# Optimization experiments

Measured on AMD Instinct MI355X. Metric: run time of the kernel, lower is better.

The kernel has to match this reference:

```python
import jax, jax.numpy as jnp
import numpy as np

B, N, E, H = 4, 512, 512, 8
HD = E // H // 2            # 32; per-head value dim is 2*HD = 64
C_IN = 64                   # u_proj Conv2d in_channels
LAMBDA_INIT = 0.8 - 0.6 * float(np.exp(-0.3 * (28.0 / 28.0) * (1 - 1)))  # layer_idx=1, depth=28 -> 0.2
LN_EPS = 1e-5


def setup_inputs() -> dict:
    key = jax.random.key(0)
    ks = jax.random.split(key, 13)
    x = jax.random.normal(ks[0], (B, N, E), dtype=jnp.float32)
    u = jax.random.normal(ks[1], (B, N, N, C_IN), dtype=jnp.float32)
    umask = jax.random.randint(ks[2], (B, N, N, 2 * H), 0, 2).astype(bool)
    s = 0.02
    v_w = jax.random.normal(ks[3], (E, E), dtype=jnp.float32) * s        # nn.Linear weight [out,in]
    out_w = jax.random.normal(ks[4], (E, E), dtype=jnp.float32) * s
    uproj_w = jax.random.normal(ks[5], (2 * H, C_IN), dtype=jnp.float32) * s  # 1x1 conv kernel
    uproj_b = jax.random.normal(ks[6], (2 * H,), dtype=jnp.float32) * s
    lq1 = jax.random.normal(ks[7], (E,), dtype=jnp.float32) * 0.1
    lk1 = jax.random.normal(ks[8], (E,), dtype=jnp.float32) * 0.1
    lq2 = jax.random.normal(ks[9], (E,), dtype=jnp.float32) * 0.1
    lk2 = jax.random.normal(ks[10], (E,), dtype=jnp.float32) * 0.1
    ln_w = jnp.ones((2 * HD,), dtype=jnp.float32)
    ln_b = jnp.zeros((2 * HD,), dtype=jnp.float32)
    return {"x": x, "u": u, "umask": umask, "v_w": v_w, "out_w": out_w,
            "uproj_w": uproj_w, "uproj_b": uproj_b,
            "lq1": lq1, "lk1": lk1, "lq2": lq2, "lk2": lk2,
            "ln_w": ln_w, "ln_b": ln_b}


def reference(x, u, umask, v_w, out_w, uproj_w, uproj_b, lq1, lk1, lq2, lk2, ln_w, ln_b):
    b, n, e = x.shape
    # v projection -> [B, H, N, 2*HD]
    v = jnp.einsum('bne,fe->bnf', x, v_w).reshape(b, n, H, 2 * HD).transpose(0, 2, 1, 3)
    # 1x1 conv on u: [B,N,N,C_IN] -> [B,N,N,2H]
    ue = jnp.einsum('bnmc,hc->bnmh', u, uproj_w) + uproj_b
    ue = jnp.where(umask, -jnp.inf, ue)
    # transpose(3,1): [B,N,N,2H] -> [B,2H,N,N]; softmax over last (key) axis
    aw = jax.nn.softmax(jnp.transpose(ue, (0, 3, 2, 1)), axis=-1)
    lam1 = jnp.exp(jnp.sum(lq1 * lk1))
    lam2 = jnp.exp(jnp.sum(lq2 * lk2))
    lam = lam1 - lam2 + LAMBDA_INIT
    aw = aw.reshape(b, H, 2, n, n)
    diff = aw[:, :, 0] - lam * aw[:, :, 1]          # [B,H,N,N]
    attn = jnp.einsum('bhnm,bhmd->bhnd', diff, v)   # [B,H,N,2HD]
    # sub-LayerNorm over last dim
    mu = jnp.mean(attn, axis=-1, keepdims=True)
    var = jnp.mean(jnp.square(attn - mu), axis=-1, keepdims=True)
    attn = (attn - mu) * jax.lax.rsqrt(var + LN_EPS) * ln_w + ln_b
    attn = attn.transpose(0, 2, 1, 3).reshape(b, n, e)
    return jnp.einsum('bne,fe->bnf', attn, out_w)
```

## Files before the change

### kernel.cpp

```cpp
#include <hip/hip_runtime.h>
#include <math.h>

typedef _Float16 f16x8 __attribute__((ext_vector_type(8)));
typedef _Float16 f16x4 __attribute__((ext_vector_type(4)));
typedef float    f32x4 __attribute__((ext_vector_type(4)));

constexpr int kB  = 4;
constexpr int kN  = 512;
constexpr int kE  = 512;
constexpr int kH  = 8;
constexpr int kH2 = 16;
constexpr int kC  = 64;
constexpr int kDV = 64;
constexpr float kLamInit = 0.2f;

__global__ __launch_bounds__(256) void prep2_kernel(
    const float* __restrict__ x, const float* __restrict__ vw,
    const float* __restrict__ ow, const int* __restrict__ umask,
    const float* __restrict__ lq1, const float* __restrict__ lk1,
    const float* __restrict__ lq2, const float* __restrict__ lk2,
    _Float16* __restrict__ x16, _Float16* __restrict__ w16v,
    _Float16* __restrict__ w16o, unsigned short* __restrict__ mbits,
    float* __restrict__ lam_out) {
  const int bid = blockIdx.x;
  if (bid < 1536) {
    const float* src; _Float16* dst; int base;
    if (bid < 1024)      { src = x;  dst = x16;  base = bid; }
    else if (bid < 1280) { src = vw; dst = w16v; base = bid - 1024; }
    else                 { src = ow; dst = w16o; base = bid - 1280; }
    const int i = base * 256 + threadIdx.x;
    const float4 v = ((const float4*)src)[i];
    union { _Float16 h[4]; uint2 u2; } P;
    P.h[0]=(_Float16)v.x; P.h[1]=(_Float16)v.y;
    P.h[2]=(_Float16)v.z; P.h[3]=(_Float16)v.w;
    *(uint2*)(dst + i * 4) = P.u2;
  } else if (bid == 1536) {
    if (threadIdx.x < 64) {
      float s1 = 0.f, s2 = 0.f;
      for (int i = threadIdx.x; i < kE; i += 64) { s1 += lq1[i]*lk1[i]; s2 += lq2[i]*lk2[i]; }
      #pragma unroll
      for (int o = 32; o; o >>= 1) { s1 += __shfl_xor(s1, o); s2 += __shfl_xor(s2, o); }
      if (threadIdx.x == 0) lam_out[0] = expf(s1) - expf(s2) + kLamInit;
    }
  } else {
    const int i = (bid - 1537) * 256 + threadIdx.x;
    const int4* src = (const int4*)(umask + (size_t)i * kH2);
    unsigned int w = 0;
    #pragma unroll
    for (int c = 0; c < 4; ++c) {
      const int4 m = src[c];
      w |= (m.x & 1) << (c * 4 + 0);
      w |= (m.y & 1) << (c * 4 + 1);
      w |= (m.z & 1) << (c * 4 + 2);
      w |= (m.w & 1) << (c * 4 + 3);
    }
    mbits[i] = (unsigned short)w;
  }
}

__global__ __launch_bounds__(256, 4) void hgemm16f2(const _Float16* __restrict__ A16,
                                                    const _Float16* __restrict__ W16,
                                                    float* __restrict__ C,
                                                    int M, int F, int K) {
  const int tid = threadIdx.x, lane = tid & 63, wv = tid >> 6;
  const int l15 = lane & 15, l4 = lane >> 4;
  const int m0 = blockIdx.y * 16;
  const int f0 = blockIdx.x * 64 + wv * 16;
  f32x4 acc = {0, 0, 0, 0};
  const _Float16* Ap = A16 + (size_t)(m0 + l15) * K + l4 * 8;
  const _Float16* Wp = W16 + (size_t)(f0 + l15) * K + l4 * 8;
  for (int k0 = 0; k0 < K; k0 += 32) {
    const f16x8 af = *(const f16x8*)(Ap + k0);
    const f16x8 bf = *(const f16x8*)(Wp + k0);
    acc = __builtin_amdgcn_mfma_f32_16x16x32_f16(af, bf, acc, 0, 0, 0);
  }
  #pragma unroll
  for (int r = 0; r < 4; ++r)
    C[(size_t)(m0 + l4 * 4 + r) * F + f0 + l15] = acc[r];
}

__global__ __launch_bounds__(256, 4) void hgemmT_v2(const _Float16* __restrict__ W16,
                                                    const _Float16* __restrict__ X16,
                                                    _Float16* __restrict__ Vt) {
  const int tid = threadIdx.x, lane = tid & 63, wv = tid >> 6;
  const int l15 = lane & 15, l4 = lane >> 4;
  const int f0 = blockIdx.y * 16;
  const int n0 = blockIdx.x * 64 + wv * 16;
  f32x4 acc = {0, 0, 0, 0};
  const _Float16* Ap = W16 + (size_t)(f0 + l15) * kE + l4 * 8;
  const _Float16* Bp = X16 + (size_t)(n0 + l15) * kE + l4 * 8;
  for (int k0 = 0; k0 < kE; k0 += 32) {
    const f16x8 af = *(const f16x8*)(Ap + k0);
    const f16x8 bf = *(const f16x8*)(Bp + k0);
    acc = __builtin_amdgcn_mfma_f32_16x16x32_f16(af, bf, acc, 0, 0, 0);
  }
  #pragma unroll
  for (int r = 0; r < 4; ++r) {
    const int f  = f0 + l4 * 4 + r;
    const int ng = n0 + l15;
    const int bb = ng >> 9, n = ng & 511;
    Vt[(((size_t)((bb * kH + (f >> 6)) * kDV) + (f & 63)) * kN) + n] = (_Float16)acc[r];
  }
}

__global__ __launch_bounds__(512, 4) void fused_attn5(
    const float* __restrict__ u, const unsigned short* __restrict__ mbits,
    const float* __restrict__ uw, const float* __restrict__ ub,
    const _Float16* __restrict__ Vt,
    _Float16* __restrict__ Opart, float* __restrict__ Spart) {
  __shared__ _Float16 P[16 * 1160];
  __shared__ float S_lds[8][16][17];
  const int tid = threadIdx.x, lane = tid & 63, wv = tid >> 6;
  const int l15 = lane & 15, l4 = lane >> 4;
  const int qt = blockIdx.x, kh = blockIdx.y, b = blockIdx.z;
  const int q0 = qt * 16;
  const int kstart = kh * 128;

  f16x8 bfrag[2];
  #pragma unroll
  for (int ch = 0; ch < 2; ++ch) {
    const float* wp = uw + l15 * 64 + ch * 32 + l4 * 8;
    const float4 wa = *(const float4*)wp;
    const float4 wb = *(const float4*)(wp + 4);
    f16x8 bf;
    bf[0]=(_Float16)wa.x; bf[1]=(_Float16)wa.y; bf[2]=(_Float16)wa.z; bf[3]=(_Float16)wa.w;
    bf[4]=(_Float16)wb.x; bf[5]=(_Float16)wb.y; bf[6]=(_Float16)wb.z; bf[7]=(_Float16)wb.w;
    bfrag[ch] = bf;
  }
  const float bias = ub[l15];

  float s_acc[4] = {};
  f32x4 oacc[2][4];
  #pragma unroll
  for (int s = 0; s < 2; ++s)
    #pragma unroll
    for (int d = 0; d < 4; ++d) oacc[s][d] = (f32x4){0,0,0,0};

  for (int t = 0; t < 2; ++t) {
    const int k0 = kstart + t * 64;
    _Float16 vals[4][8];
    #pragma unroll
    for (int kk = 0; kk < 8; ++kk) {
      const int k = k0 + wv * 8 + kk;
      const float* up = u + (((size_t)(b * kN + k)) * kN + q0 + l15) * kC + l4 * 8;
      f32x4 acc = {0.f, 0.f, 0.f, 0.f};
      #pragma unroll
      for (int ch = 0; ch < 2; ++ch) {
        const float4 a0 = *(const float4*)(up + ch * 32);
        const float4 a1 = *(const float4*)(up + ch * 32 + 4);
        f16x8 af;
        af[0]=(_Float16)a0.x; af[1]=(_Float16)a0.y; af[2]=(_Float16)a0.z; af[3]=(_Float16)a0.w;
        af[4]=(_Float16)a1.x; af[5]=(_Float16)a1.y; af[6]=(_Float16)a1.z; af[7]=(_Float16)a1.w;
        acc = __builtin_amdgcn_mfma_f32_16x16x32_f16(af, bfrag[ch], acc, 0, 0, 0);
      }
      const unsigned long long w64 =
          *(const unsigned long long*)(mbits + ((size_t)(b * kN + k)) * kN + q0 + l4 * 4);
      #pragma unroll
      for (int r = 0; r < 4; ++r) {
        const float e = ((w64 >> (r * 16 + l15)) & 1ULL) ? 0.f : __expf(acc[r] + bias);
        s_acc[r] += e;
        vals[r][kk] = (_Float16)e;
      }
    }
    #pragma unroll
    for (int r = 0; r < 4; ++r) {
      union { _Float16 h[8]; int4 v; } PK;
      #pragma unroll
      for (int kk = 0; kk < 8; ++kk) PK.h[kk] = vals[r][kk];
      *(int4*)&P[l15 * 1160 + (l4 * 4 + r) * 72 + wv * 8] = PK.v;
    }
    __syncthreads();
    f16x8 va[2][4];
    #pragma unroll
    for (int hf = 0; hf < 2; ++hf)
      #pragma unroll
      for (int dt = 0; dt < 4; ++dt)
        va[hf][dt] = *(const f16x8*)(Vt + (((size_t)((b * kH + wv) * kDV + dt * 16 + l15)) * kN)
                                     + k0 + hf * 32 + l4 * 8);
    #pragma unroll
    for (int s = 0; s < 2; ++s) {
      #pragma unroll
      for (int hf = 0; hf < 2; ++hf) {
        const f16x8 pb = *(const f16x8*)&P[(wv * 2 + s) * 1160 + l15 * 72 + hf * 32 + l4 * 8];
        #pragma unroll
        for (int dt = 0; dt < 4; ++dt)
          oacc[s][dt] = __builtin_amdgcn_mfma_f32_16x16x32_f16(va[hf][dt], pb, oacc[s][dt], 0, 0, 0);
      }
    }
    __syncthreads();
  }

  #pragma unroll
  for (int r = 0; r < 4; ++r) S_lds[wv][l15][l4 * 4 + r] = s_acc[r];
  __syncthreads();
  const int blk = (b * 4 + kh) * 32 + qt;
  if (tid < 256) {
    const int h2 = tid >> 4, q = tid & 15;
    float S = 0.f;
    #pragma unroll
    for (int j = 0; j < 8; ++j) S += S_lds[j][h2][q];
    Spart[(size_t)blk * 256 + h2 * 16 + q] = S;
  }
  _Float16* ob = Opart + (size_t)blk * 16384;
  #pragma unroll
  for (int s = 0; s < 2; ++s)
    #pragma unroll
    for (int dt = 0; dt < 4; ++dt)
      #pragma unroll
      for (int r = 0; r < 4; ++r)
        ob[((size_t)(s * 8 + wv) * 64 + dt * 16 + l4 * 4 + r) * 16 + l15] =
            (_Float16)oacc[s][dt][r];
}

__global__ __launch_bounds__(256) void combine3(
    const _Float16* __restrict__ Opart, const float* __restrict__ Spart,
    const float* __restrict__ lam_p, const float* __restrict__ ln_w,
    const float* __restrict__ ln_b, _Float16* __restrict__ a16) {
  __shared__ float vsh[64][17];
  __shared__ float inv_sh[2][16];
  const int tid = threadIdx.x;
  const int qt = blockIdx.x, h = blockIdx.y, b = blockIdx.z;
  if (tid < 32) {
    const int s = tid >> 4, q = tid & 15;
    float S = 0.f;
    #pragma unroll
    for (int kh = 0; kh < 4; ++kh)
      S += Spart[(size_t)((b * 4 + kh) * 32 + qt) * 256 + (h * 2 + s) * 16 + q];
    inv_sh[s][q] = (s ? lam_p[0] : 1.0f) / S;
  }
  float a0[4] = {}, a1[4] = {};
  #pragma unroll
  for (int kh = 0; kh < 4; ++kh) {
    const size_t base = (size_t)((b * 4 + kh) * 32 + qt) * 16384;
    const f16x4 p0 = *(const f16x4*)(Opart + base + (size_t)(0 * 8 + h) * 1024 + tid * 4);
    const f16x4 p1 = *(const f16x4*)(Opart + base + (size_t)(1 * 8 + h) * 1024 + tid * 4);
    #pragma unroll
    for (int j = 0; j < 4; ++j) { a0[j] += (float)p0[j]; a1[j] += (float)p1[j]; }
  }
  __syncthreads();
  {
    const int d = tid >> 2, q0i = (tid & 3) * 4;
    #pragma unroll
    for (int j = 0; j < 4; ++j)
      vsh[d][q0i + j] = a0[j] * inv_sh[0][q0i + j] - a1[j] * inv_sh[1][q0i + j];
  }
  __syncthreads();
  const int q = tid >> 4, i = tid & 15;
  float vv[4], s1 = 0.f, s2 = 0.f;
  #pragma unroll
  for (int jj = 0; jj < 4; ++jj) {
    vv[jj] = vsh[i * 4 + jj][q];
    s1 += vv[jj]; s2 += vv[jj] * vv[jj];
  }
  #pragma unroll
  for (int o = 1; o < 16; o <<= 1) { s1 += __shfl_xor(s1, o); s2 += __shfl_xor(s2, o); }
  const float mu = s1 * (1.0f / kDV);
  const float var = s2 * (1.0f / kDV) - mu * mu;
  const float rstd = rsqrtf(var + 1e-5f);
  union { _Float16 hh[4]; uint2 u2; } PK;
  #pragma unroll
  for (int jj = 0; jj < 4; ++jj)
    PK.hh[jj] = (_Float16)((vv[jj] - mu) * rstd * ln_w[i * 4 + jj] + ln_b[i * 4 + jj]);
  *(uint2*)(a16 + ((size_t)(b * kN + qt * 16 + q)) * kE + h * kDV + i * 4) = PK.u2;
}

extern "C" void kernel_launch(void* const* d_in, const int* in_sizes, int n_in,
                              void* d_out, int out_size, void* d_ws, size_t ws_size,
                              hipStream_t stream) {
  const float* x     = (const float*)d_in[0];
  const float* u     = (const float*)d_in[1];
  const int*   umask = (const int*)d_in[2];
  const float* v_w   = (const float*)d_in[3];
  const float* out_w = (const float*)d_in[4];
  const float* uw    = (const float*)d_in[5];
  const float* ubias = (const float*)d_in[6];
  const float* lq1   = (const float*)d_in[7];
  const float* lk1   = (const float*)d_in[8];
  const float* lq2   = (const float*)d_in[9];
  const float* lk2   = (const float*)d_in[10];
  const float* ln_w  = (const float*)d_in[11];
  const float* ln_b  = (const float*)d_in[12];
  float* out = (float*)d_out;

  char* ws = (char*)d_ws;
  const size_t sz_half = (size_t)kB * kN * kE * 2;
  const size_t sz_w16  = (size_t)kE * kE * 2;
  const size_t sz_op   = (size_t)512 * 16384 * 2;
  const size_t sz_sp   = (size_t)512 * 256 * 4;
  const size_t sz_mb   = (size_t)kB * kN * kN * 2;
  const size_t off_x16 = 256;
  const size_t off_wv  = off_x16 + sz_half;
  const size_t off_wo  = off_wv + sz_w16;
  const size_t off_vt  = off_wo + sz_w16;
  const size_t off_a16 = off_vt + sz_half;
  const size_t off_op  = off_a16 + sz_half;
  const size_t off_sp  = off_op + sz_op;
  const size_t off_mb  = off_sp + sz_sp;
  if (ws_size < off_mb + sz_mb) return;
  float*    lam   = (float*)(ws);
  _Float16* x16   = (_Float16*)(ws + off_x16);
  _Float16* w16v  = (_Float16*)(ws + off_wv);
  _Float16* w16o  = (_Float16*)(ws + off_wo);
  _Float16* Vt    = (_Float16*)(ws + off_vt);
  _Float16* a16   = (_Float16*)(ws + off_a16);
  _Float16* Opart = (_Float16*)(ws + off_op);
  float*    Spart = (float*)(ws + off_sp);
  unsigned short* mbits = (unsigned short*)(ws + off_mb);

  prep2_kernel<<<dim3(5633), dim3(256), 0, stream>>>(
      x, v_w, out_w, umask, lq1, lk1, lq2, lk2, x16, w16v, w16o, mbits, lam);
  hgemmT_v2<<<dim3(32, 32), dim3(256), 0, stream>>>(w16v, x16, Vt);
  fused_attn5<<<dim3(kN / 16, 4, kB), dim3(512), 0, stream>>>(
      u, mbits, uw, ubias, Vt, Opart, Spart);
  combine3<<<dim3(kN / 16, kH, kB), dim3(256), 0, stream>>>(
      Opart, Spart, lam, ln_w, ln_b, a16);
  hgemm16f2<<<dim3(kE / 64, (kB * kN) / 16), dim3(256), 0, stream>>>(
      a16, w16o, out, kB * kN, kE, kE);
}
```

Before: 122.1 us.

## Split key range eight ways in fused attention and pack fp16 conversions

The fused attention kernel now splits the key dimension into 8 chunks instead of 4, halving per-block work and LDS footprint, and the launch bounds request more resident blocks. This doubles the grid to expose more parallelism and occupancy on the u-streaming stage. In exchange, the partial output and sum buffers double, and the combine kernel reads twice as many partials. Float-to-half conversions also switch to packed round-toward-zero cvt_pkrtz, which cuts instruction count but changes the rounding mode.

```diff
diff --git a/kernel.cpp b/kernel.cpp
--- a/kernel.cpp
+++ b/kernel.cpp
@@ -3,7 +3,13 @@
 
 typedef _Float16 f16x8 __attribute__((ext_vector_type(8)));
 typedef _Float16 f16x4 __attribute__((ext_vector_type(4)));
+typedef __fp16   h16x2 __attribute__((ext_vector_type(2)));
 typedef float    f32x4 __attribute__((ext_vector_type(4)));
+
+static __device__ __forceinline__ unsigned int pkrtz(float a, float b) {
+  const h16x2 p = __builtin_amdgcn_cvt_pkrtz(a, b);
+  return __builtin_bit_cast(unsigned int, p);
+}
 
 constexpr int kB  = 4;
 constexpr int kN  = 512;
@@ -30,10 +36,10 @@
     else                 { src = ow; dst = w16o; base = bid - 1280; }
     const int i = base * 256 + threadIdx.x;
     const float4 v = ((const float4*)src)[i];
-    union { _Float16 h[4]; uint2 u2; } P;
-    P.h[0]=(_Float16)v.x; P.h[1]=(_Float16)v.y;
-    P.h[2]=(_Float16)v.z; P.h[3]=(_Float16)v.w;
-    *(uint2*)(dst + i * 4) = P.u2;
+    uint2 P;
+    P.x = pkrtz(v.x, v.y);
+    P.y = pkrtz(v.z, v.w);
+    *(uint2*)(dst + i * 4) = P;
   } else if (bid == 1536) {
     if (threadIdx.x < 64) {
       float s1 = 0.f, s2 = 0.f;
@@ -103,18 +109,18 @@
   }
 }
 
-__global__ __launch_bounds__(512, 4) void fused_attn5(
+__global__ __launch_bounds__(512, 6) void fused_attn6(
     const float* __restrict__ u, const unsigned short* __restrict__ mbits,
     const float* __restrict__ uw, const float* __restrict__ ub,
     const _Float16* __restrict__ Vt,
     _Float16* __restrict__ Opart, float* __restrict__ Spart) {
-  __shared__ _Float16 P[16 * 1160];
+  __shared__ _Float16 P[16 * 648];
   __shared__ float S_lds[8][16][17];
   const int tid = threadIdx.x, lane = tid & 63, wv = tid >> 6;
   const int l15 = lane & 15, l4 = lane >> 4;
   const int qt = blockIdx.x, kh = blockIdx.y, b = blockIdx.z;
   const int q0 = qt * 16;
-  const int kstart = kh * 128;
+  const int kstart = kh * 64;
 
   f16x8 bfrag[2];
   #pragma unroll
@@ -122,10 +128,12 @@
     const float* wp = uw + l15 * 64 + ch * 32 + l4 * 8;
     const float4 wa = *(const float4*)wp;
     const float4 wb = *(const float4*)(wp + 4);
-    f16x8 bf;
-    bf[0]=(_Float16)wa.x; bf[1]=(_Float16)wa.y; bf[2]=(_Float16)wa.z; bf[3]=(_Float16)wa.w;
-    bf[4]=(_Float16)wb.x; bf[5]=(_Float16)wb.y; bf[6]=(_Float16)wb.z; bf[7]=(_Float16)wb.w;
-    bfrag[ch] = bf;
+    union { unsigned int u[4]; f16x8 v; } BF;
+    BF.u[0] = pkrtz(wa.x, wa.y);
+    BF.u[1] = pkrtz(wa.z, wa.w);
+    BF.u[2] = pkrtz(wb.x, wb.y);
+    BF.u[3] = pkrtz(wb.z, wb.w);
+    bfrag[ch] = BF.v;
   }
   const float bias = ub[l15];
 
@@ -137,21 +145,24 @@
     for (int d = 0; d < 4; ++d) oacc[s][d] = (f32x4){0,0,0,0};
 
   for (int t = 0; t < 2; ++t) {
-    const int k0 = kstart + t * 64;
-    _Float16 vals[4][8];
-    #pragma unroll
-    for (int kk = 0; kk < 8; ++kk) {
-      const int k = k0 + wv * 8 + kk;
+    const int k0 = kstart + t * 32;
+    float ep0[4];
+    unsigned int pk0[4], pk1[4];
+    #pragma unroll
+    for (int kk = 0; kk < 4; ++kk) {
+      const int k = k0 + wv * 4 + kk;
       const float* up = u + (((size_t)(b * kN + k)) * kN + q0 + l15) * kC + l4 * 8;
       f32x4 acc = {0.f, 0.f, 0.f, 0.f};
       #pragma unroll
       for (int ch = 0; ch < 2; ++ch) {
         const float4 a0 = *(const float4*)(up + ch * 32);
         const float4 a1 = *(const float4*)(up + ch * 32 + 4);
-        f16x8 af;
-        af[0]=(_Float16)a0.x; af[1]=(_Float16)a0.y; af[2]=(_Float16)a0.z; af[3]=(_Float16)a0.w;
-        af[4]=(_Float16)a1.x; af[5]=(_Float16)a1.y; af[6]=(_Float16)a1.z; af[7]=(_Float16)a1.w;
-        acc = __builtin_amdgcn_mfma_f32_16x16x32_f16(af, bfrag[ch], acc, 0, 0, 0);
+        union { unsigned int u[4]; f16x8 v; } AF;
+        AF.u[0] = pkrtz(a0.x, a0.y);
+        AF.u[1] = pkrtz(a0.z, a0.w);
+        AF.u[2] = pkrtz(a1.x, a1.y);
+        AF.u[3] = pkrtz(a1.z, a1.w);
+        acc = __builtin_amdgcn_mfma_f32_16x16x32_f16(AF.v, bfrag[ch], acc, 0, 0, 0);
       }
       const unsigned long long w64 =
           *(const unsigned long long*)(mbits + ((size_t)(b * kN + k)) * kN + q0 + l4 * 4);
@@ -159,32 +170,29 @@
       for (int r = 0; r < 4; ++r) {
         const float e = ((w64 >> (r * 16 + l15)) & 1ULL) ? 0.f : __expf(acc[r] + bias);
         s_acc[r] += e;
-        vals[r][kk] = (_Float16)e;
+        if ((kk & 1) == 0) {
+          ep0[r] = e;
+        } else {
+          const unsigned int pp = pkrtz(ep0[r], e);
+          if (kk == 1) pk0[r] = pp;
+          else         pk1[r] = pp;
+        }
       }
     }
     #pragma unroll
     for (int r = 0; r < 4; ++r) {
-      union { _Float16 h[8]; int4 v; } PK;
-      #pragma unroll
-      for (int kk = 0; kk < 8; ++kk) PK.h[kk] = vals[r][kk];
-      *(int4*)&P[l15 * 1160 + (l4 * 4 + r) * 72 + wv * 8] = PK.v;
+      uint2 w; w.x = pk0[r]; w.y = pk1[r];
+      *(uint2*)&P[l15 * 648 + (l4 * 4 + r) * 40 + wv * 4] = w;
     }
     __syncthreads();
-    f16x8 va[2][4];
-    #pragma unroll
-    for (int hf = 0; hf < 2; ++hf)
-      #pragma unroll
-      for (int dt = 0; dt < 4; ++dt)
-        va[hf][dt] = *(const f16x8*)(Vt + (((size_t)((b * kH + wv) * kDV + dt * 16 + l15)) * kN)
-                                     + k0 + hf * 32 + l4 * 8);
-    #pragma unroll
-    for (int s = 0; s < 2; ++s) {
-      #pragma unroll
-      for (int hf = 0; hf < 2; ++hf) {
-        const f16x8 pb = *(const f16x8*)&P[(wv * 2 + s) * 1160 + l15 * 72 + hf * 32 + l4 * 8];
-        #pragma unroll
-        for (int dt = 0; dt < 4; ++dt)
-          oacc[s][dt] = __builtin_amdgcn_mfma_f32_16x16x32_f16(va[hf][dt], pb, oacc[s][dt], 0, 0, 0);
+    #pragma unroll
+    for (int dt = 0; dt < 4; ++dt) {
+      const f16x8 va = *(const f16x8*)(Vt +
+          (((size_t)((b * kH + wv) * kDV + dt * 16 + l15)) * kN) + k0 + l4 * 8);
+      #pragma unroll
+      for (int s = 0; s < 2; ++s) {
+        const f16x8 pb = *(const f16x8*)&P[(wv * 2 + s) * 648 + l15 * 40 + l4 * 8];
+        oacc[s][dt] = __builtin_amdgcn_mfma_f32_16x16x32_f16(va, pb, oacc[s][dt], 0, 0, 0);
       }
     }
     __syncthreads();
@@ -193,7 +201,7 @@
   #pragma unroll
   for (int r = 0; r < 4; ++r) S_lds[wv][l15][l4 * 4 + r] = s_acc[r];
   __syncthreads();
-  const int blk = (b * 4 + kh) * 32 + qt;
+  const int blk = (b * 8 + kh) * 32 + qt;
   if (tid < 256) {
     const int h2 = tid >> 4, q = tid & 15;
     float S = 0.f;
@@ -224,14 +232,14 @@
     const int s = tid >> 4, q = tid & 15;
     float S = 0.f;
     #pragma unroll
-    for (int kh = 0; kh < 4; ++kh)
-      S += Spart[(size_t)((b * 4 + kh) * 32 + qt) * 256 + (h * 2 + s) * 16 + q];
+    for (int kh = 0; kh < 8; ++kh)
+      S += Spart[(size_t)((b * 8 + kh) * 32 + qt) * 256 + (h * 2 + s) * 16 + q];
     inv_sh[s][q] = (s ? lam_p[0] : 1.0f) / S;
   }
   float a0[4] = {}, a1[4] = {};
   #pragma unroll
-  for (int kh = 0; kh < 4; ++kh) {
-    const size_t base = (size_t)((b * 4 + kh) * 32 + qt) * 16384;
+  for (int kh = 0; kh < 8; ++kh) {
+    const size_t base = (size_t)((b * 8 + kh) * 32 + qt) * 16384;
     const f16x4 p0 = *(const f16x4*)(Opart + base + (size_t)(0 * 8 + h) * 1024 + tid * 4);
     const f16x4 p1 = *(const f16x4*)(Opart + base + (size_t)(1 * 8 + h) * 1024 + tid * 4);
     #pragma unroll
@@ -285,8 +293,8 @@
   char* ws = (char*)d_ws;
   const size_t sz_half = (size_t)kB * kN * kE * 2;
   const size_t sz_w16  = (size_t)kE * kE * 2;
-  const size_t sz_op   = (size_t)512 * 16384 * 2;
-  const size_t sz_sp   = (size_t)512 * 256 * 4;
+  const size_t sz_op   = (size_t)1024 * 16384 * 2;
+  const size_t sz_sp   = (size_t)1024 * 256 * 4;
   const size_t sz_mb   = (size_t)kB * kN * kN * 2;
   const size_t off_x16 = 256;
   const size_t off_wv  = off_x16 + sz_half;
@@ -310,7 +318,7 @@
   prep2_kernel<<<dim3(5633), dim3(256), 0, stream>>>(
       x, v_w, out_w, umask, lq1, lk1, lq2, lk2, x16, w16v, w16o, mbits, lam);
   hgemmT_v2<<<dim3(32, 32), dim3(256), 0, stream>>>(w16v, x16, Vt);
-  fused_attn5<<<dim3(kN / 16, 4, kB), dim3(512), 0, stream>>>(
+  fused_attn6<<<dim3(kN / 16, 8, kB), dim3(512), 0, stream>>>(
       u, mbits, uw, ubias, Vt, Opart, Spart);
   combine3<<<dim3(kN / 16, kH, kB), dim3(256), 0, stream>>>(
       Opart, Spart, lam, ln_w, ln_b, a16);
```

Measured after the change: 153.2 us. 1.26x slower.
